# Performance work log

Measured on AMD Instinct MI355X. Metric: run time of the kernel, lower is better.

Reference implementation:

```python
import jax, jax.numpy as jnp
import numpy as np

N = 50000      # nodes
D = 256        # input_features
K = 64         # hiddens (per-head out dim)
H = 8          # nheads
O = 64         # outputs
E = 1600000    # edges
ALPHA = 0.2    # leaky-relu negative slope


def setup_inputs() -> dict:
    key = jax.random.key(0)
    ks = jax.random.split(key, 8)
    x = jax.random.normal(ks[0], (N, D), dtype=jnp.float32)
    edges = jax.random.randint(ks[1], (2, E), 0, N, dtype=jnp.int64)
    layer_W = jax.random.normal(ks[2], (D, D), dtype=jnp.float32) * (1.0 / np.sqrt(D))
    layer_b = jnp.zeros((D,), dtype=jnp.float32)
    heads_W = jax.random.normal(ks[3], (H, D, K), dtype=jnp.float32) * (1.0 / np.sqrt(D))
    heads_a = jax.random.normal(ks[4], (H, 2 * K), dtype=jnp.float32) * 0.1
    end_W = jax.random.normal(ks[5], (H * K, O), dtype=jnp.float32) * (1.0 / np.sqrt(H * K))
    end_a = jax.random.normal(ks[6], (2 * O,), dtype=jnp.float32) * 0.1
    return {"x": x, "edges": edges, "layer_W": layer_W, "layer_b": layer_b,
            "heads_W": heads_W, "heads_a": heads_a, "end_W": end_W, "end_a": end_a}


def _gat_layer(x, W, a, src, dst):
    # x: [N, Din], W: [Din, Dout], a: [2*Dout]
    h = x @ W                                    # [N, Dout]
    k = h.shape[1]
    # a . [h_src || h_dst] == (h @ a_src)[src] + (h @ a_dst)[dst]  (cheap: project then gather scalars)
    s = (h @ a[:k])[src] + (h @ a[k:])[dst]      # [E]
    e = jax.nn.leaky_relu(s, ALPHA)
    # numerically-stable segment softmax over edges grouped by destination node
    m = jax.ops.segment_max(e, dst, num_segments=N)        # [N]
    w = jnp.exp(e - m[dst])                                # [E]
    denom = jax.ops.segment_sum(w, dst, num_segments=N)    # [N]
    attn = w / (denom[dst] + 1e-16)                        # [E]
    out = jax.ops.segment_sum(attn[:, None] * h[src], dst, num_segments=N)  # [N, Dout]
    return jax.nn.elu(out)


def reference(x, edges, layer_W, layer_b, heads_W, heads_a, end_W, end_a):
    src, dst = edges[0], edges[1]
    x = x @ layer_W + layer_b                    # nn.Linear(input_features, input_features)
    # multi-head sparse attention, concat over heads -> [N, H*K]
    hcat = jnp.concatenate(
        [_gat_layer(x, heads_W[i], heads_a[i], src, dst) for i in range(H)], axis=1)
    out = _gat_layer(hcat, end_W, end_a, src, dst)  # [N, O]
    return jax.nn.softmax(out, axis=1)
```

## Files before the change

kernel.cpp:

```cpp
#include <hip/hip_runtime.h>
#include <math.h>

#define NN 50000
#define DD 256
#define KK 64
#define HH 8
#define OO 64
#define EE 1600000
#define LRELU_ALPHA 0.2f
#define HK 512
#define NX 640
#define N3 80

typedef __attribute__((ext_vector_type(8))) short short8;
typedef __attribute__((ext_vector_type(4))) float floatx4;

__device__ inline void bsplit(float f, unsigned short& h, unsigned short& l) {
    unsigned u = __float_as_uint(f);
    h = (unsigned short)(u >> 16);
    float fh = __uint_as_float(u & 0xffff0000u);
    l = (unsigned short)(__float_as_uint(f - fh) >> 16);
}

__global__ void pack_heads_kernel(const float* __restrict__ hw, float* __restrict__ Bp) {
    int t = blockIdx.x * 256 + threadIdx.x;
    if (t >= HH * DD * KK) return;
    int h = t >> 14;
    int r = t & 16383;
    int d = r >> 6;
    int k = r & 63;
    Bp[d * HK + h * KK + k] = hw[t];
}

__global__ void bias_pack_kernel(const float* __restrict__ b, const float* __restrict__ Bp,
                                 float* __restrict__ bc) {
    int c = blockIdx.x * 256 + threadIdx.x;
    if (c >= HK) return;
    float s = 0.f;
    for (int d = 0; d < DD; d++) s += b[d] * Bp[d * HK + c];
    bc[c] = s;
}

__global__ void build_wext_kernel(const float* __restrict__ Wc, const float* __restrict__ heads_a,
                                  unsigned short* __restrict__ Th, unsigned short* __restrict__ Tl) {
    int t = blockIdx.x * 256 + threadIdx.x;
    int col = t >> 8, d = t & 255;
    if (col >= NX) return;
    float v = 0.f;
    if (col < HK) {
        v = Wc[d * HK + col];
    } else if (col < HK + 8) {
        int h = col - HK;
        for (int k = 0; k < 64; k++) v += Wc[d * HK + h * 64 + k] * heads_a[h * 128 + k];
    } else if (col < HK + 16) {
        int h = col - HK - 8;
        for (int k = 0; k < 64; k++) v += Wc[d * HK + h * 64 + k] * heads_a[h * 128 + 64 + k];
    }
    unsigned short hi, lo;
    bsplit(v, hi, lo);
    Th[(size_t)col * DD + d] = hi;
    Tl[(size_t)col * DD + d] = lo;
}

__global__ void bias_ext_kernel(const float* __restrict__ bc, const float* __restrict__ heads_a,
                                float* __restrict__ be) {
    int c = blockIdx.x * 256 + threadIdx.x;
    if (c >= NX) return;
    float v = 0.f;
    if (c < HK) v = bc[c];
    else if (c < HK + 8) {
        int h = c - HK;
        for (int k = 0; k < 64; k++) v += bc[h * 64 + k] * heads_a[h * 128 + k];
    } else if (c < HK + 16) {
        int h = c - HK - 8;
        for (int k = 0; k < 64; k++) v += bc[h * 64 + k] * heads_a[h * 128 + 64 + k];
    }
    be[c] = v;
}

__global__ void build_eext_kernel(const float* __restrict__ eW, const float* __restrict__ ea,
                                  unsigned short* __restrict__ Th, unsigned short* __restrict__ Tl) {
    int t = blockIdx.x * 256 + threadIdx.x;
    int col = t >> 9, k = t & 511;
    if (col >= N3) return;
    float v = 0.f;
    if (col < OO) v = eW[(size_t)k * OO + col];
    else if (col == OO) { for (int j = 0; j < OO; j++) v += eW[(size_t)k * OO + j] * ea[j]; }
    else if (col == OO + 1) { for (int j = 0; j < OO; j++) v += eW[(size_t)k * OO + j] * ea[64 + j]; }
    unsigned short hi, lo;
    bsplit(v, hi, lo);
    Th[(size_t)col * HK + k] = hi;
    Tl[(size_t)col * HK + k] = lo;
}

__global__ void split_x_kernel(const float* __restrict__ x, unsigned short* __restrict__ xh,
                               unsigned short* __restrict__ xl) {
    int t = blockIdx.x * 256 + threadIdx.x;
    if (t >= NN * 64) return;
    float4 v = ((const float4*)x)[t];
    ushort4 vh, vl;
    bsplit(v.x, vh.x, vl.x);
    bsplit(v.y, vh.y, vl.y);
    bsplit(v.z, vh.z, vl.z);
    bsplit(v.w, vh.w, vl.w);
    ((ushort4*)xh)[t] = vh;
    ((ushort4*)xl)[t] = vl;
}

#define GM 128
#define GN 128
#define GKT 16
__global__ __launch_bounds__(256) void sgemm128_kernel(
    const float* __restrict__ A, const float* __restrict__ B,
    const float* __restrict__ bias, float* __restrict__ C,
    int M, int N, int K)
{
    __shared__ float As[GKT][GM + 4];
    __shared__ float Bs[GKT][GN + 4];
    int tid = threadIdx.x;
    int row0 = blockIdx.y * GM, col0 = blockIdx.x * GN;
    int tx = tid & 15, ty = tid >> 4;
    int ar = tid >> 1;
    int ac0 = (tid & 1) * 8;
    float acc[8][8] = {};
    for (int k0 = 0; k0 < K; k0 += GKT) {
#pragma unroll
        for (int i = 0; i < 2; i++) {
            int gr = row0 + ar;
            int gc = k0 + ac0 + i * 4;
            float4 v = make_float4(0.f, 0.f, 0.f, 0.f);
            if (gr < M) v = *(const float4*)&A[(size_t)gr * K + gc];
            As[ac0 + i * 4 + 0][ar] = v.x;
            As[ac0 + i * 4 + 1][ar] = v.y;
            As[ac0 + i * 4 + 2][ar] = v.z;
            As[ac0 + i * 4 + 3][ar] = v.w;
        }
#pragma unroll
        for (int i = 0; i < 2; i++) {
            int idx = tid + i * 256;
            int br = idx >> 5;
            int bc = (idx & 31) * 4;
            float4 v = make_float4(0.f, 0.f, 0.f, 0.f);
            int gc = col0 + bc;
            if (gc < N) v = *(const float4*)&B[(size_t)(k0 + br) * N + gc];
            *(float4*)&Bs[br][bc] = v;
        }
        __syncthreads();
#pragma unroll
        for (int k = 0; k < GKT; k++) {
            float4 a0 = *(const float4*)&As[k][ty * 4];
            float4 a1 = *(const float4*)&As[k][64 + ty * 4];
            float4 b0 = *(const float4*)&Bs[k][tx * 4];
            float4 b1 = *(const float4*)&Bs[k][64 + tx * 4];
            float av[8] = {a0.x, a0.y, a0.z, a0.w, a1.x, a1.y, a1.z, a1.w};
            float bv[8] = {b0.x, b0.y, b0.z, b0.w, b1.x, b1.y, b1.z, b1.w};
#pragma unroll
            for (int i = 0; i < 8; i++)
#pragma unroll
                for (int j = 0; j < 8; j++) acc[i][j] += av[i] * bv[j];
        }
        __syncthreads();
    }
#pragma unroll
    for (int i = 0; i < 8; i++) {
        int gr = row0 + (i < 4 ? ty * 4 + i : 64 + ty * 4 + i - 4);
        if (gr >= M) continue;
#pragma unroll
        for (int j = 0; j < 8; j++) {
            int gc = col0 + (j < 4 ? tx * 4 + j : 64 + tx * 4 + j - 4);
            if (gc >= N) continue;
            float v = acc[i][j];
            if (bias) v += bias[gc];
            C[(size_t)gr * N + gc] = v;
        }
    }
}

#define LDA 40
__global__ __launch_bounds__(256) void mfma_gemm1_kernel(
    const unsigned short* __restrict__ xh, const unsigned short* __restrict__ xl,
    const unsigned short* __restrict__ BhT, const unsigned short* __restrict__ BlT,
    const float* __restrict__ bias_ext,
    float* __restrict__ Hh_t, float* __restrict__ ssrc_t, float* __restrict__ sdst_t)
{
    __shared__ unsigned short AhL[128 * LDA];
    __shared__ unsigned short AlL[128 * LDA];
    __shared__ unsigned short BhL[128 * LDA];
    __shared__ unsigned short BlL[128 * LDA];
    int tid = threadIdx.x, widx = tid >> 6, lane = tid & 63;
    int row0 = blockIdx.y * 128, col0 = blockIdx.x * 128;
    int wrow = (widx >> 1) * 64, wcol = (widx & 1) * 64;
    int lrow = lane & 15, lq = lane >> 4;
    int sr = tid >> 1;
    int sc = (tid & 1) * 16;
    floatx4 acc[4][4] = {};
    for (int k0 = 0; k0 < DD; k0 += 32) {
        int gr = row0 + sr;
        if (gr < NN) {
            size_t ab = (size_t)gr * DD + k0 + sc;
            *(uint4*)&AhL[sr * LDA + sc]     = *(const uint4*)&xh[ab];
            *(uint4*)&AhL[sr * LDA + sc + 8] = *(const uint4*)&xh[ab + 8];
            *(uint4*)&AlL[sr * LDA + sc]     = *(const uint4*)&xl[ab];
            *(uint4*)&AlL[sr * LDA + sc + 8] = *(const uint4*)&xl[ab + 8];
        } else {
            uint4 z = {0, 0, 0, 0};
            *(uint4*)&AhL[sr * LDA + sc] = z;     *(uint4*)&AhL[sr * LDA + sc + 8] = z;
            *(uint4*)&AlL[sr * LDA + sc] = z;     *(uint4*)&AlL[sr * LDA + sc + 8] = z;
        }
        size_t bb = (size_t)(col0 + sr) * DD + k0 + sc;
        *(uint4*)&BhL[sr * LDA + sc]     = *(const uint4*)&BhT[bb];
        *(uint4*)&BhL[sr * LDA + sc + 8] = *(const uint4*)&BhT[bb + 8];
        *(uint4*)&BlL[sr * LDA + sc]     = *(const uint4*)&BlT[bb];
        *(uint4*)&BlL[sr * LDA + sc + 8] = *(const uint4*)&BlT[bb + 8];
        __syncthreads();
        short8 ah[4], al[4], bh[4], bl[4];
#pragma unroll
        for (int mi = 0; mi < 4; mi++) {
            int r = wrow + mi * 16 + lrow;
            ah[mi] = *(const short8*)&AhL[r * LDA + lq * 8];
            al[mi] = *(const short8*)&AlL[r * LDA + lq * 8];
        }
#pragma unroll
        for (int ni = 0; ni < 4; ni++) {
            int c = wcol + ni * 16 + lrow;
            bh[ni] = *(const short8*)&BhL[c * LDA + lq * 8];
            bl[ni] = *(const short8*)&BlL[c * LDA + lq * 8];
        }
#pragma unroll
        for (int mi = 0; mi < 4; mi++)
#pragma unroll
            for (int ni = 0; ni < 4; ni++) {
                acc[mi][ni] = __builtin_amdgcn_mfma_f32_16x16x32_bf16(al[mi], bh[ni], acc[mi][ni], 0, 0, 0);
                acc[mi][ni] = __builtin_amdgcn_mfma_f32_16x16x32_bf16(ah[mi], bl[ni], acc[mi][ni], 0, 0, 0);
                acc[mi][ni] = __builtin_amdgcn_mfma_f32_16x16x32_bf16(ah[mi], bh[ni], acc[mi][ni], 0, 0, 0);
            }
        __syncthreads();
    }
#pragma unroll
    for (int mi = 0; mi < 4; mi++)
#pragma unroll
        for (int ni = 0; ni < 4; ni++)
#pragma unroll
            for (int r = 0; r < 4; r++) {
                int grow = row0 + wrow + mi * 16 + lq * 4 + r;
                int gcol = col0 + wcol + ni * 16 + lrow;
                if (grow < NN && gcol < HK + 16) {
                    float v = acc[mi][ni][r] + bias_ext[gcol];
                    if (gcol < HK)
                        Hh_t[((size_t)(gcol >> 6) * NN + grow) * 64 + (gcol & 63)] = v;
                    else if (gcol < HK + 8)
                        ssrc_t[(size_t)(gcol - HK) * NN + grow] = v;
                    else
                        sdst_t[(size_t)(gcol - HK - 8) * NN + grow] = v;
                }
            }
}

__global__ __launch_bounds__(256) void mfma_gemm3_kernel(
    const unsigned short* __restrict__ hch, const unsigned short* __restrict__ hcl,
    const unsigned short* __restrict__ BhT, const unsigned short* __restrict__ BlT,
    float* __restrict__ h2, float* __restrict__ s2src, float* __restrict__ s2dst)
{
    __shared__ unsigned short AhL[64 * LDA];
    __shared__ unsigned short AlL[64 * LDA];
    __shared__ unsigned short BhL[N3 * LDA];
    __shared__ unsigned short BlL[N3 * LDA];
    int tid = threadIdx.x, widx = tid >> 6, lane = tid & 63;
    int row0 = blockIdx.x * 64;
    int wrow = widx * 16;
    int lrow = lane & 15, lq = lane >> 4;
    int sr = tid >> 2;
    int sc = (tid & 3) * 8;
    floatx4 acc[5] = {};
    for (int k0 = 0; k0 < HK; k0 += 32) {
        int gr = row0 + sr;
        if (gr < NN) {
            size_t ab = (size_t)gr * HK + k0 + sc;
            *(uint4*)&AhL[sr * LDA + sc] = *(const uint4*)&hch[ab];
            *(uint4*)&AlL[sr * LDA + sc] = *(const uint4*)&hcl[ab];
        } else {
            uint4 z = {0, 0, 0, 0};
            *(uint4*)&AhL[sr * LDA + sc] = z;
            *(uint4*)&AlL[sr * LDA + sc] = z;
        }
#pragma unroll
        for (int i = 0; i < 2; i++) {
            int idx = tid + i * 256;
            if (idx < N3 * 4) {
                int r = idx >> 2, c8 = (idx & 3) * 8;
                size_t bb = (size_t)r * HK + k0 + c8;
                *(uint4*)&BhL[r * LDA + c8] = *(const uint4*)&BhT[bb];
                *(uint4*)&BlL[r * LDA + c8] = *(const uint4*)&BlT[bb];
            }
        }
        __syncthreads();
        short8 ah, al, bh[5], bl[5];
        int r = wrow + lrow;
        ah = *(const short8*)&AhL[r * LDA + lq * 8];
        al = *(const short8*)&AlL[r * LDA + lq * 8];
#pragma unroll
        for (int ni = 0; ni < 5; ni++) {
            int c = ni * 16 + lrow;
            bh[ni] = *(const short8*)&BhL[c * LDA + lq * 8];
            bl[ni] = *(const short8*)&BlL[c * LDA + lq * 8];
        }
#pragma unroll
        for (int ni = 0; ni < 5; ni++) {
            acc[ni] = __builtin_amdgcn_mfma_f32_16x16x32_bf16(al, bh[ni], acc[ni], 0, 0, 0);
            acc[ni] = __builtin_amdgcn_mfma_f32_16x16x32_bf16(ah, bl[ni], acc[ni], 0, 0, 0);
            acc[ni] = __builtin_amdgcn_mfma_f32_16x16x32_bf16(ah, bh[ni], acc[ni], 0, 0, 0);
        }
        __syncthreads();
    }
#pragma unroll
    for (int ni = 0; ni < 5; ni++)
#pragma unroll
        for (int r = 0; r < 4; r++) {
            int grow = row0 + wrow + lq * 4 + r;
            int gcol = ni * 16 + lrow;
            if (grow < NN) {
                float v = acc[ni][r];
                if (gcol < OO) h2[(size_t)grow * OO + gcol] = v;
                else if (gcol == OO) s2src[grow] = v;
                else if (gcol == OO + 1) s2dst[grow] = v;
            }
        }
}

__global__ void hist_kernel(const int* __restrict__ dst, int* __restrict__ deg) {
    int t = blockIdx.x * 256 + threadIdx.x;
    if (t < EE) atomicAdd(&deg[dst[t]], 1);
}

__global__ void scan1_kernel(const int* __restrict__ deg, int* __restrict__ part,
                             int* __restrict__ bsum) {
    __shared__ int ws_[4];
    int i = blockIdx.x * 256 + threadIdx.x;
    int lane = threadIdx.x & 63, wv = threadIdx.x >> 6;
    int v = (i < NN) ? deg[i] : 0;
    int x = v;
#pragma unroll
    for (int d = 1; d < 64; d <<= 1) {
        int t = __shfl_up(x, d, 64);
        if (lane >= d) x += t;
    }
    if (lane == 63) ws_[wv] = x;
    __syncthreads();
    int add = 0;
    for (int k = 0; k < wv; k++) add += ws_[k];
    x += add;
    if (i < NN) part[i] = x;
    if (threadIdx.x == 255) bsum[blockIdx.x] = x;
}

__global__ void scan2_kernel(int* __restrict__ bsum, int nb) {
    __shared__ int ws_[4];
    int tid = threadIdx.x;
    int lane = tid & 63, wv = tid >> 6;
    int v = (tid < nb) ? bsum[tid] : 0;
    int x = v;
#pragma unroll
    for (int d = 1; d < 64; d <<= 1) {
        int t = __shfl_up(x, d, 64);
        if (lane >= d) x += t;
    }
    if (lane == 63) ws_[wv] = x;
    __syncthreads();
    int add = 0;
    for (int k = 0; k < wv; k++) add += ws_[k];
    x += add;
    if (tid < nb) bsum[tid] = x;
}

__global__ void scan3_kernel(const int* __restrict__ deg, const int* __restrict__ part,
                             const int* __restrict__ bsum, int* __restrict__ offs,
                             int* __restrict__ cursor) {
    int i = blockIdx.x * 256 + threadIdx.x;
    if (i >= NN) return;
    int carry = blockIdx.x ? bsum[blockIdx.x - 1] : 0;
    int incl = part[i] + carry;
    offs[i + 1] = incl;
    cursor[i] = incl - deg[i];
    if (i == 0) offs[0] = 0;
}

__global__ void scatter_kernel(const int* __restrict__ src, const int* __restrict__ dst,
                               int* __restrict__ cursor, int* __restrict__ ssorted) {
    int t = blockIdx.x * 256 + threadIdx.x;
    if (t < EE) {
        int d = dst[t];
        int pos = atomicAdd(&cursor[d], 1);
        ssorted[pos] = src[t];
    }
}

#define AP 8
__global__ __launch_bounds__(256) void agg_heads_kernel(
    const float* __restrict__ Hh_t, const float* __restrict__ ssrc_t,
    const float* __restrict__ sdst_t, const int* __restrict__ offs,
    const int* __restrict__ ssorted,
    unsigned short* __restrict__ hch, unsigned short* __restrict__ hcl)
{
    __shared__ int2 sSW[4][64];
    int wv = threadIdx.x >> 6, lane = threadIdx.x & 63;
    int w = blockIdx.x * 4 + wv;
    if (w >= NN * HH) return;
    int h = w / NN, n = w - h * NN;
    const char* Hsb = (const char*)(Hh_t + (size_t)h * NN * 64);
    const float* srcs = ssrc_t + (size_t)h * NN;
    int beg = offs[n], deg = offs[n + 1] - beg;
    int g = lane >> 4, q = lane & 15;
    int qoff = q * 16;
    float4 acc = make_float4(0.f, 0.f, 0.f, 0.f);
    float den = 0.f;
    float sd = (deg > 0) ? sdst_t[(size_t)h * NN + n] : 0.f;
    for (int c0 = 0; c0 < deg; c0 += 64) {
        int jj = c0 + lane;
        int s = 0;
        float wgt = 0.f;
        if (jj < deg) {
            s = ssorted[beg + jj];
            float sv = srcs[s] + sd;
            float e = (sv >= 0.f) ? sv : LRELU_ALPHA * sv;
            wgt = __expf(e);
        }
        den += wgt;
        sSW[wv][lane] = make_int2(s << 8, __float_as_int(wgt));
        int clen = min(64, deg - c0);
        int nbat = (clen + 31) >> 5;
        for (int b = 0; b < nbat; b++) {
            int base = b * AP;
            int soff[AP];
            float wb[AP];
#pragma unroll
            for (int p2 = 0; p2 < AP; p2++) {
                int2 t2 = sSW[wv][(base + p2) * 4 + g];
                soff[p2] = t2.x;
                wb[p2] = __int_as_float(t2.y);
            }
            float4 vb[AP];
#pragma unroll
            for (int p2 = 0; p2 < AP; p2++)
                vb[p2] = *(const float4*)(Hsb + soff[p2] + qoff);
#pragma unroll
            for (int p2 = 0; p2 < AP; p2++) {
                acc.x += wb[p2] * vb[p2].x;
                acc.y += wb[p2] * vb[p2].y;
                acc.z += wb[p2] * vb[p2].z;
                acc.w += wb[p2] * vb[p2].w;
            }
        }
    }
#pragma unroll
    for (int off = 32; off; off >>= 1) den += __shfl_xor(den, off, 64);
#pragma unroll
    for (int off = 16; off < 64; off <<= 1) {
        acc.x += __shfl_xor(acc.x, off, 64);
        acc.y += __shfl_xor(acc.y, off, 64);
        acc.z += __shfl_xor(acc.z, off, 64);
        acc.w += __shfl_xor(acc.w, off, 64);
    }
    if (g == 0) {
        float inv = 1.f / (den + 1e-16f);
        float r0 = acc.x * inv, r1 = acc.y * inv, r2 = acc.z * inv, r3 = acc.w * inv;
        r0 = (r0 > 0.f) ? r0 : (__expf(r0) - 1.f);
        r1 = (r1 > 0.f) ? r1 : (__expf(r1) - 1.f);
        r2 = (r2 > 0.f) ? r2 : (__expf(r2) - 1.f);
        r3 = (r3 > 0.f) ? r3 : (__expf(r3) - 1.f);
        ushort4 vh, vl;
        bsplit(r0, vh.x, vl.x);
        bsplit(r1, vh.y, vl.y);
        bsplit(r2, vh.z, vl.z);
        bsplit(r3, vh.w, vl.w);
        size_t o = (size_t)n * HK + h * 64 + q * 4;
        unsigned long long ph =
            (unsigned long long)vh.x | ((unsigned long long)vh.y << 16) |
            ((unsigned long long)vh.z << 32) | ((unsigned long long)vh.w << 48);
        unsigned long long pl =
            (unsigned long long)vl.x | ((unsigned long long)vl.y << 16) |
            ((unsigned long long)vl.z << 32) | ((unsigned long long)vl.w << 48);
        __builtin_nontemporal_store(ph, (unsigned long long*)&hch[o]);
        __builtin_nontemporal_store(pl, (unsigned long long*)&hcl[o]);
    }
}

__global__ __launch_bounds__(256) void agg_final_kernel(
    const float* __restrict__ h2, const float* __restrict__ s2src,
    const float* __restrict__ s2dst, const int* __restrict__ offs,
    const int* __restrict__ ssorted, float* __restrict__ out)
{
    __shared__ int2 sSW[4][64];
    int wv = threadIdx.x >> 6, lane = threadIdx.x & 63;
    int n = blockIdx.x * 4 + wv;
    if (n >= NN) return;
    int beg = offs[n], deg = offs[n + 1] - beg;
    int g = lane >> 4, q = lane & 15;
    int qoff = q * 16;
    const char* h2b = (const char*)h2;
    float4 acc = make_float4(0.f, 0.f, 0.f, 0.f);
    float den = 0.f;
    float sd = (deg > 0) ? s2dst[n] : 0.f;
    for (int c0 = 0; c0 < deg; c0 += 64) {
        int jj = c0 + lane;
        int s = 0;
        float wgt = 0.f;
        if (jj < deg) {
            s = ssorted[beg + jj];
            float sv = s2src[s] + sd;
            float e = (sv >= 0.f) ? sv : LRELU_ALPHA * sv;
            wgt = __expf(e);
        }
        den += wgt;
        sSW[wv][lane] = make_int2(s << 8, __float_as_int(wgt));
        int clen = min(64, deg - c0);
        int nbat = (clen + 31) >> 5;
        for (int b = 0; b < nbat; b++) {
            int base = b * AP;
            int soff[AP];
            float wb[AP];
#pragma unroll
            for (int p2 = 0; p2 < AP; p2++) {
                int2 t2 = sSW[wv][(base + p2) * 4 + g];
                soff[p2] = t2.x;
                wb[p2] = __int_as_float(t2.y);
            }
            float4 vb[AP];
#pragma unroll
            for (int p2 = 0; p2 < AP; p2++)
                vb[p2] = *(const float4*)(h2b + soff[p2] + qoff);
#pragma unroll
            for (int p2 = 0; p2 < AP; p2++) {
                acc.x += wb[p2] * vb[p2].x;
                acc.y += wb[p2] * vb[p2].y;
                acc.z += wb[p2] * vb[p2].z;
                acc.w += wb[p2] * vb[p2].w;
            }
        }
    }
#pragma unroll
    for (int off = 32; off; off >>= 1) den += __shfl_xor(den, off, 64);
#pragma unroll
    for (int off = 16; off < 64; off <<= 1) {
        acc.x += __shfl_xor(acc.x, off, 64);
        acc.y += __shfl_xor(acc.y, off, 64);
        acc.z += __shfl_xor(acc.z, off, 64);
        acc.w += __shfl_xor(acc.w, off, 64);
    }
    float inv = 1.f / (den + 1e-16f);
    float r0 = acc.x * inv, r1 = acc.y * inv, r2 = acc.z * inv, r3 = acc.w * inv;
    r0 = (r0 > 0.f) ? r0 : (__expf(r0) - 1.f);
    r1 = (r1 > 0.f) ? r1 : (__expf(r1) - 1.f);
    r2 = (r2 > 0.f) ? r2 : (__expf(r2) - 1.f);
    r3 = (r3 > 0.f) ? r3 : (__expf(r3) - 1.f);
    float mm = fmaxf(fmaxf(r0, r1), fmaxf(r2, r3));
#pragma unroll
    for (int off = 1; off < 16; off <<= 1) mm = fmaxf(mm, __shfl_xor(mm, off, 64));
    float p0 = __expf(r0 - mm), p1 = __expf(r1 - mm);
    float p2 = __expf(r2 - mm), p3 = __expf(r3 - mm);
    float sum = p0 + p1 + p2 + p3;
#pragma unroll
    for (int off = 1; off < 16; off <<= 1) sum += __shfl_xor(sum, off, 64);
    float is = 1.f / sum;
    if (g == 0) {
        float4 res = make_float4(p0 * is, p1 * is, p2 * is, p3 * is);
        *(float4*)&out[(size_t)n * OO + q * 4] = res;
    }
}

extern "C" void kernel_launch(void* const* d_in, const int* in_sizes, int n_in,
                              void* d_out, int out_size, void* d_ws, size_t ws_size,
                              hipStream_t stream) {
    const float* x       = (const float*)d_in[0];
    const int*   edges   = (const int*)d_in[1];
    const float* layer_W = (const float*)d_in[2];
    const float* layer_b = (const float*)d_in[3];
    const float* heads_W = (const float*)d_in[4];
    const float* heads_a = (const float*)d_in[5];
    const float* end_W   = (const float*)d_in[6];
    const float* end_a   = (const float*)d_in[7];
    float* out = (float*)d_out;

    const int* src = edges;
    const int* dst = edges + EE;

    char* ws = (char*)d_ws;
    size_t wsp = 0;
    auto alloc = [&](size_t bytes) -> void* {
        void* r = ws + wsp;
        wsp += (bytes + 255) & ~(size_t)255;
        return r;
    };
    float* Hh_t  = (float*)alloc((size_t)NN * HK * 4);
    unsigned short* hch = (unsigned short*)alloc((size_t)NN * HK * 2);
    unsigned short* hcl = (unsigned short*)alloc((size_t)NN * HK * 2);
    float* h2    = (float*)alloc((size_t)NN * OO * 4);
    float* Bp    = (float*)alloc((size_t)DD * HK * 4);
    float* Wc    = (float*)alloc((size_t)DD * HK * 4);
    float* bc    = (float*)alloc((size_t)HK * 4);
    unsigned short* WexthT = (unsigned short*)alloc((size_t)NX * DD * 2);
    unsigned short* WextlT = (unsigned short*)alloc((size_t)NX * DD * 2);
    unsigned short* eexthT = (unsigned short*)alloc((size_t)N3 * HK * 2);
    unsigned short* eextlT = (unsigned short*)alloc((size_t)N3 * HK * 2);
    float* bias_ext = (float*)alloc((size_t)NX * 4);
    float* ssrc_t = (float*)alloc((size_t)HH * NN * 4);
    float* sdst_t = (float*)alloc((size_t)HH * NN * 4);
    float* s2src = (float*)alloc((size_t)NN * 4);
    float* s2dst = (float*)alloc((size_t)NN * 4);
    int* deg     = (int*)alloc((size_t)NN * 4);
    int* offs    = (int*)alloc((size_t)(NN + 1) * 4);
    int* cursor  = (int*)alloc((size_t)NN * 4);
    int* part    = (int*)alloc((size_t)NN * 4);
    int* bsum    = (int*)alloc((size_t)256 * 4);
    int* ssorted = (int*)alloc((size_t)EE * 4);

    unsigned short* xh = hch;
    unsigned short* xl = hcl;

    const int NB = (NN + 255) / 256;

    (void)hipMemsetAsync(deg, 0, (size_t)NN * 4, stream);

    pack_heads_kernel<<<(HH * DD * KK + 255) / 256, 256, 0, stream>>>(heads_W, Bp);
    bias_pack_kernel<<<2, 256, 0, stream>>>(layer_b, Bp, bc);
    sgemm128_kernel<<<dim3(HK / GN, DD / GM), 256, 0, stream>>>(
        layer_W, Bp, nullptr, Wc, DD, HK, DD);
    build_wext_kernel<<<(NX * DD + 255) / 256, 256, 0, stream>>>(Wc, heads_a, WexthT, WextlT);
    bias_ext_kernel<<<(NX + 255) / 256, 256, 0, stream>>>(bc, heads_a, bias_ext);
    build_eext_kernel<<<(N3 * HK + 255) / 256, 256, 0, stream>>>(end_W, end_a, eexthT, eextlT);
    split_x_kernel<<<(NN * 64 + 255) / 256, 256, 0, stream>>>(x, xh, xl);

    mfma_gemm1_kernel<<<dim3(NX / 128, (NN + 127) / 128), 256, 0, stream>>>(
        xh, xl, WexthT, WextlT, bias_ext, Hh_t, ssrc_t, sdst_t);

    hist_kernel<<<(EE + 255) / 256, 256, 0, stream>>>(dst, deg);
    scan1_kernel<<<NB, 256, 0, stream>>>(deg, part, bsum);
    scan2_kernel<<<1, 256, 0, stream>>>(bsum, NB);
    scan3_kernel<<<NB, 256, 0, stream>>>(deg, part, bsum, offs, cursor);
    scatter_kernel<<<(EE + 255) / 256, 256, 0, stream>>>(src, dst, cursor, ssorted);

    agg_heads_kernel<<<(NN * HH + 3) / 4, 256, 0, stream>>>(
        Hh_t, ssrc_t, sdst_t, offs, ssorted, hch, hcl);

    mfma_gemm3_kernel<<<(NN + 63) / 64, 256, 0, stream>>>(
        hch, hcl, eexthT, eextlT, h2, s2src, s2dst);

    agg_final_kernel<<<(NN + 3) / 4, 256, 0, stream>>>(h2, s2src, s2dst, offs, ssorted, out);
}
```

Before: 957.6 us.

## Register-prefetch next K tile in GEMMs and shrink aggregation batch size

Both MFMA GEMM kernels now load the next K-slice from global memory into registers right after the barrier, so those loads overlap the MFMA work on the current tile before being written to shared memory. Row bounds checks are replaced by clamping out-of-range rows to row 0, which reads valid but unused data. Separately, the edge-aggregation kernels halve the gather batch (AP 8 to 4) with matching batch counts. This reduces per-batch padding for low-degree nodes and register pressure, at the cost of fewer loads in flight per batch. The prefetch raises register use in the GEMMs.

Result: no change. 943.6 us (-1.5%).

```diff
diff --git a/kernel.cpp b/kernel.cpp
--- a/kernel.cpp
+++ b/kernel.cpp
@@ -193,26 +193,35 @@
     int lrow = lane & 15, lq = lane >> 4;
     int sr = tid >> 1;
     int sc = (tid & 1) * 16;
+    int gr = row0 + sr;
+    size_t abase = (gr < NN) ? (size_t)gr * DD : 0;
+    size_t bbase = (size_t)(col0 + sr) * DD;
     floatx4 acc[4][4] = {};
+    uint4 pah0, pah1, pal0, pal1, pbh0, pbh1, pbl0, pbl1;
+    {
+        size_t ab = abase + sc, bb = bbase + sc;
+        pah0 = *(const uint4*)&xh[ab];   pah1 = *(const uint4*)&xh[ab + 8];
+        pal0 = *(const uint4*)&xl[ab];   pal1 = *(const uint4*)&xl[ab + 8];
+        pbh0 = *(const uint4*)&BhT[bb];  pbh1 = *(const uint4*)&BhT[bb + 8];
+        pbl0 = *(const uint4*)&BlT[bb];  pbl1 = *(const uint4*)&BlT[bb + 8];
+    }
     for (int k0 = 0; k0 < DD; k0 += 32) {
-        int gr = row0 + sr;
-        if (gr < NN) {
-            size_t ab = (size_t)gr * DD + k0 + sc;
-            *(uint4*)&AhL[sr * LDA + sc]     = *(const uint4*)&xh[ab];
-            *(uint4*)&AhL[sr * LDA + sc + 8] = *(const uint4*)&xh[ab + 8];
-            *(uint4*)&AlL[sr * LDA + sc]     = *(const uint4*)&xl[ab];
-            *(uint4*)&AlL[sr * LDA + sc + 8] = *(const uint4*)&xl[ab + 8];
-        } else {
-            uint4 z = {0, 0, 0, 0};
-            *(uint4*)&AhL[sr * LDA + sc] = z;     *(uint4*)&AhL[sr * LDA + sc + 8] = z;
-            *(uint4*)&AlL[sr * LDA + sc] = z;     *(uint4*)&AlL[sr * LDA + sc + 8] = z;
-        }
-        size_t bb = (size_t)(col0 + sr) * DD + k0 + sc;
-        *(uint4*)&BhL[sr * LDA + sc]     = *(const uint4*)&BhT[bb];
-        *(uint4*)&BhL[sr * LDA + sc + 8] = *(const uint4*)&BhT[bb + 8];
-        *(uint4*)&BlL[sr * LDA + sc]     = *(const uint4*)&BlT[bb];
-        *(uint4*)&BlL[sr * LDA + sc + 8] = *(const uint4*)&BlT[bb + 8];
+        *(uint4*)&AhL[sr * LDA + sc]     = pah0;
+        *(uint4*)&AhL[sr * LDA + sc + 8] = pah1;
+        *(uint4*)&AlL[sr * LDA + sc]     = pal0;
+        *(uint4*)&AlL[sr * LDA + sc + 8] = pal1;
+        *(uint4*)&BhL[sr * LDA + sc]     = pbh0;
+        *(uint4*)&BhL[sr * LDA + sc + 8] = pbh1;
+        *(uint4*)&BlL[sr * LDA + sc]     = pbl0;
+        *(uint4*)&BlL[sr * LDA + sc + 8] = pbl1;
         __syncthreads();
+        if (k0 + 32 < DD) {
+            size_t ab = abase + k0 + 32 + sc, bb = bbase + k0 + 32 + sc;
+            pah0 = *(const uint4*)&xh[ab];   pah1 = *(const uint4*)&xh[ab + 8];
+            pal0 = *(const uint4*)&xl[ab];   pal1 = *(const uint4*)&xl[ab + 8];
+            pbh0 = *(const uint4*)&BhT[bb];  pbh1 = *(const uint4*)&BhT[bb + 8];
+            pbl0 = *(const uint4*)&BlT[bb];  pbl1 = *(const uint4*)&BlT[bb + 8];
+        }
         short8 ah[4], al[4], bh[4], bl[4];
 #pragma unroll
         for (int mi = 0; mi < 4; mi++) {
@@ -271,29 +280,46 @@
     int lrow = lane & 15, lq = lane >> 4;
     int sr = tid >> 2;
     int sc = (tid & 3) * 8;
+    int gr = row0 + sr;
+    size_t abase = (gr < NN) ? (size_t)gr * HK : 0;
+    int bidx0 = tid;
+    int br0 = bidx0 >> 2, bc0 = (bidx0 & 3) * 8;
+    int bidx1 = tid + 256;
+    bool b1ok = (bidx1 < N3 * 4);
+    int br1 = bidx1 >> 2, bc1 = (bidx1 & 3) * 8;
     floatx4 acc[5] = {};
+    uint4 pa0, pa1, pb0h, pb0l, pb1h, pb1l;
+    {
+        pa0 = *(const uint4*)&hch[abase + sc];
+        pa1 = *(const uint4*)&hcl[abase + sc];
+        pb0h = *(const uint4*)&BhT[(size_t)br0 * HK + bc0];
+        pb0l = *(const uint4*)&BlT[(size_t)br0 * HK + bc0];
+        if (b1ok) {
+            pb1h = *(const uint4*)&BhT[(size_t)br1 * HK + bc1];
+            pb1l = *(const uint4*)&BlT[(size_t)br1 * HK + bc1];
+        }
+    }
     for (int k0 = 0; k0 < HK; k0 += 32) {
-        int gr = row0 + sr;
-        if (gr < NN) {
-            size_t ab = (size_t)gr * HK + k0 + sc;
-            *(uint4*)&AhL[sr * LDA + sc] = *(const uint4*)&hch[ab];
-            *(uint4*)&AlL[sr * LDA + sc] = *(const uint4*)&hcl[ab];
-        } else {
-            uint4 z = {0, 0, 0, 0};
-            *(uint4*)&AhL[sr * LDA + sc] = z;
-            *(uint4*)&AlL[sr * LDA + sc] = z;
-        }
-#pragma unroll
-        for (int i = 0; i < 2; i++) {
-            int idx = tid + i * 256;
-            if (idx < N3 * 4) {
-                int r = idx >> 2, c8 = (idx & 3) * 8;
-                size_t bb = (size_t)r * HK + k0 + c8;
-                *(uint4*)&BhL[r * LDA + c8] = *(const uint4*)&BhT[bb];
-                *(uint4*)&BlL[r * LDA + c8] = *(const uint4*)&BlT[bb];
-            }
+        *(uint4*)&AhL[sr * LDA + sc] = pa0;
+        *(uint4*)&AlL[sr * LDA + sc] = pa1;
+        *(uint4*)&BhL[br0 * LDA + bc0] = pb0h;
+        *(uint4*)&BlL[br0 * LDA + bc0] = pb0l;
+        if (b1ok) {
+            *(uint4*)&BhL[br1 * LDA + bc1] = pb1h;
+            *(uint4*)&BlL[br1 * LDA + bc1] = pb1l;
         }
         __syncthreads();
+        if (k0 + 32 < HK) {
+            size_t ab = abase + k0 + 32 + sc;
+            pa0 = *(const uint4*)&hch[ab];
+            pa1 = *(const uint4*)&hcl[ab];
+            pb0h = *(const uint4*)&BhT[(size_t)br0 * HK + k0 + 32 + bc0];
+            pb0l = *(const uint4*)&BlT[(size_t)br0 * HK + k0 + 32 + bc0];
+            if (b1ok) {
+                pb1h = *(const uint4*)&BhT[(size_t)br1 * HK + k0 + 32 + bc1];
+                pb1l = *(const uint4*)&BlT[(size_t)br1 * HK + k0 + 32 + bc1];
+            }
+        }
         short8 ah, al, bh[5], bl[5];
         int r = wrow + lrow;
         ah = *(const short8*)&AhL[r * LDA + lq * 8];
@@ -394,7 +420,7 @@
     }
 }
 
-#define AP 8
+#define AP 4
 __global__ __launch_bounds__(256) void agg_heads_kernel(
     const float* __restrict__ Hh_t, const float* __restrict__ ssrc_t,
     const float* __restrict__ sdst_t, const int* __restrict__ offs,
@@ -427,7 +453,7 @@
         den += wgt;
         sSW[wv][lane] = make_int2(s << 8, __float_as_int(wgt));
         int clen = min(64, deg - c0);
-        int nbat = (clen + 31) >> 5;
+        int nbat = (clen + 15) >> 4;
         for (int b = 0; b < nbat; b++) {
             int base = b * AP;
             int soff[AP];
@@ -513,7 +539,7 @@
         den += wgt;
         sSW[wv][lane] = make_int2(s << 8, __float_as_int(wgt));
         int clen = min(64, deg - c0);
-        int nbat = (clen + 31) >> 5;
+        int nbat = (clen + 15) >> 4;
         for (int b = 0; b < nbat; b++) {
             int base = b * AP;
             int soff[AP];
```
